# Optimization experiments

Measured on AMD Instinct MI355X. Metric: run time of the kernel, lower is better.

## Reference

```python
import jax, jax.numpy as jnp
import numpy as np
from jax import lax

K = 3          # kernel size
STRIDE = 1
PAD = 1
DIL = 1


def conv2d(x, w, b, stride, pad):
    y = lax.conv_general_dilated(
        x, w, (stride, stride), [(pad, pad), (pad, pad)],
        dimension_numbers=('NCHW', 'OIHW', 'NCHW'))
    return y + b[None, :, None, None]


def deform_conv2d(x, offset, mask, weight, bias):
    # x: [B,C,H,W]; offset: [B,2*K*K,Ho,Wo] (channel 2i = y_i, 2i+1 = x_i);
    # mask: [B,K*K,Ho,Wo]; weight: [Cout,C,K,K]  (deformable_groups=1, groups=1)
    B, C, H, W = x.shape
    Ho, Wo = offset.shape[2], offset.shape[3]
    KK = K * K
    off = offset.reshape(B, KK, 2, Ho, Wo)
    off_y, off_x = off[:, :, 0], off[:, :, 1]          # [B,KK,Ho,Wo]

    ky, kx = jnp.meshgrid(jnp.arange(K), jnp.arange(K), indexing='ij')
    ky, kx = ky.ravel(), kx.ravel()                    # [KK]
    base_y = (jnp.arange(Ho) * STRIDE - PAD)[None, :, None] + (ky * DIL)[:, None, None]
    base_x = (jnp.arange(Wo) * STRIDE - PAD)[None, None, :] + (kx * DIL)[:, None, None]
    py = base_y[None].astype(x.dtype) + off_y          # [B,KK,Ho,Wo]
    px = base_x[None].astype(x.dtype) + off_x

    y0 = jnp.floor(py)
    x0 = jnp.floor(px)
    ly = py - y0
    lx = px - x0
    y0i = y0.astype(jnp.int32)
    x0i = x0.astype(jnp.int32)
    y1i = y0i + 1
    x1i = x0i + 1

    x_flat = x.reshape(B, C, H * W)

    def gather(yi, xi):
        valid = (yi >= 0) & (yi < H) & (xi >= 0) & (xi < W)
        idx = jnp.clip(yi, 0, H - 1) * W + jnp.clip(xi, 0, W - 1)
        v = jax.vmap(lambda xb, ib: xb[:, ib])(x_flat, idx.reshape(B, -1))
        v = v.reshape(B, C, KK, Ho, Wo)
        return v * valid[:, None].astype(x.dtype)

    w00 = ((1 - ly) * (1 - lx))[:, None]
    w01 = ((1 - ly) * lx)[:, None]
    w10 = (ly * (1 - lx))[:, None]
    w11 = (ly * lx)[:, None]
    samp = (w00 * gather(y0i, x0i) + w01 * gather(y0i, x1i)
            + w10 * gather(y1i, x0i) + w11 * gather(y1i, x1i))  # [B,C,KK,Ho,Wo]

    mod = samp * mask[:, None]                          # modulated samples
    wr = weight.reshape(weight.shape[0], C, KK)
    out = jnp.einsum('ocp,bcphw->bohw', wr, mod)
    return out + bias[None, :, None, None]


def setup_inputs() -> dict:
    key = jax.random.key(0)
    k1, k2, k3, k4, k5 = jax.random.split(key, 5)
    B, Cin, Cout, H, W = 4, 64, 128, 128, 128
    x = jax.random.normal(k1, (B, Cin, H, W), dtype=jnp.float32)
    # offset/mask conv: 3*K*K channels (o1, o2, mask). Zero-init in the source;
    # small random values here so nonzero offsets exercise the gather.
    offset_w = jax.random.normal(k2, (3 * K * K, Cin, K, K), dtype=jnp.float32) * 0.01
    offset_b = jax.random.normal(k3, (3 * K * K,), dtype=jnp.float32) * 0.01
    weight = jax.random.normal(k4, (Cout, Cin, K, K), dtype=jnp.float32) * (1.0 / np.sqrt(Cin * K * K))
    bias = jax.random.normal(k5, (Cout,), dtype=jnp.float32) * 0.01
    return {'x': x, 'offset_w': offset_w, 'offset_b': offset_b, 'weight': weight, 'bias': bias}


def reference(x, offset_w, offset_b, weight, bias):
    out = conv2d(x, offset_w, offset_b, STRIDE, PAD)    # [B,3*KK,Ho,Wo]
    o1, o2, m = jnp.split(out, 3, axis=1)
    offset = jnp.concatenate([o1, o2], axis=1)          # [B,2*KK,Ho,Wo]
    mask = jax.nn.sigmoid(m)                            # [B,KK,Ho,Wo]
    return deform_conv2d(x, offset, mask, weight, bias)
```

## Files before the change

### kernel.cpp

```cpp
#include <hip/hip_runtime.h>
#include <math.h>

#define HH   128
#define WW   128
#define HWP  16384
#define CIN  64
#define COUT 128

typedef float  f32x4  __attribute__((ext_vector_type(4)));
typedef short  short8 __attribute__((ext_vector_type(8)));

#define WBF_B   ((size_t)0)
#define OWBF_B  ((size_t)147456)
#define XT_B    ((size_t)221184)
#define WS_NEED ((size_t)8609792)

__device__ inline unsigned short f2bf(float f) {
    unsigned u = __builtin_bit_cast(unsigned, f);
    return (unsigned short)((u + 0x7FFFu + ((u >> 16) & 1u)) >> 16);
}

__global__ __launch_bounds__(256) void k_prep(const float* __restrict__ x,
                                              const float* __restrict__ wgt,
                                              const float* __restrict__ ow,
                                              unsigned short* __restrict__ xt,
                                              unsigned short* __restrict__ wbf,
                                              unsigned short* __restrict__ owbf) {
    int t = threadIdx.x;
    if (blockIdx.x < 2048) {
        int cgrp = t & 7, px = t >> 3;
        int pix = blockIdx.x * 32 + px;
        int b = pix >> 14, hw = pix & 16383;
        const float* xp = x + (size_t)b * CIN * HWP + (size_t)(cgrp * 8) * HWP + hw;
        unsigned pk[4];
#pragma unroll
        for (int d = 0; d < 4; ++d) {
            float lo = xp[(size_t)(2 * d) * HWP];
            float hi = xp[(size_t)(2 * d + 1) * HWP];
            pk[d] = (unsigned)f2bf(lo) | ((unsigned)f2bf(hi) << 16);
        }
        *(uint4*)(xt + (size_t)pix * 64 + cgrp * 8) = *(uint4*)pk;
    } else {
        int tid = (blockIdx.x - 2048) * 256 + t;
        {
            int oc = tid / 576;
            int r  = tid - oc * 576;
            int kk = r >> 6;
            int c  = r & 63;
            wbf[tid] = f2bf(wgt[((size_t)oc * CIN + c) * 9 + kk]);
        }
        if (tid < 32 * 576) {
            int oc  = tid / 576;
            int r   = tid - oc * 576;
            int tap = r >> 6;
            int c   = r & 63;
            owbf[tid] = (oc < 27) ? f2bf(ow[((size_t)oc * CIN + c) * 9 + tap]) : 0;
        }
    }
}

__global__ __launch_bounds__(256) void k_fused_v2(const unsigned short* __restrict__ xt,
                                                  const unsigned short* __restrict__ wbf,
                                                  const unsigned short* __restrict__ owbf,
                                                  const float* __restrict__ ob,
                                                  const float* __restrict__ bias,
                                                  float* __restrict__ out) {
    __shared__ __align__(16) char smem[11648];
    char*  mbase  = smem;
    float* meta_s = (float*)(smem + 8192);

    int blk0 = blockIdx.x;
    int blk  = (blk0 & 7) * 256 + (blk0 >> 3);
    int b   = blk >> 9;
    int rem = blk & 511;
    int h   = rem >> 2;
    int w0  = (rem & 3) << 5;
    int t   = threadIdx.x;

    int p1 = t >> 3;
    int cg = t & 7;
    int l  = t & 63;
    int wid = t >> 6;
    int lm = l & 15, lk = l >> 4;

    const unsigned short* xbt = xt + (size_t)b * HWP * 64;

    int ocf = wid >> 1, pxf = wid & 1;
    int spx = pxf * 16 + lm;
    f32x4 sacc = {0.f, 0.f, 0.f, 0.f};
    const unsigned short* sab = owbf + (size_t)(ocf * 16 + lm) * 576 + lk * 8;

#pragma unroll
    for (int tap = 0; tap < 9; ++tap) {
        int ky = tap / 3, kx = tap % 3;
        int yy = h - 1 + ky;
        int xx = w0 - 1 + kx + spx;
        bool vld = (yy >= 0) && (yy < HH) && (xx >= 0) && (xx < WW);
        int yc = min(max(yy, 0), HH - 1), xc = min(max(xx, 0), WW - 1);
        const unsigned short* bp = xbt + (size_t)(yc * WW + xc) * 64 + lk * 8;
#pragma unroll
        for (int ch = 0; ch < 2; ++ch) {
            short8 a = *(const short8*)(sab + tap * 64 + ch * 32);
            uint4 v = *(const uint4*)(bp + ch * 32);
            v.x = vld ? v.x : 0u;  v.y = vld ? v.y : 0u;
            v.z = vld ? v.z : 0u;  v.w = vld ? v.w : 0u;
            sacc = __builtin_amdgcn_mfma_f32_16x16x32_bf16(a, __builtin_bit_cast(short8, v), sacc, 0, 0, 0);
        }
    }
#pragma unroll
    for (int r = 0; r < 4; ++r) {
        int oc = ocf * 16 + lk * 4 + r;
        if (oc < 27) {
            float v = sacc[r] + ob[oc];
            if (oc < 18) {
                meta_s[(oc & 1) * 288 + (oc >> 1) * 32 + spx] = v;
            } else {
                meta_s[2 * 288 + (oc - 18) * 32 + spx] = 1.f / (1.f + expf(-v));
            }
        }
    }
    __syncthreads();

    f32x4 acc00 = {0.f,0.f,0.f,0.f};
    f32x4 acc01 = {0.f,0.f,0.f,0.f};
    f32x4 acc10 = {0.f,0.f,0.f,0.f};
    f32x4 acc11 = {0.f,0.f,0.f,0.f};

    const unsigned short* arow0 = wbf + (size_t)(wid * 32 + lm) * 576 + lk * 8;
    const unsigned short* arow1 = arow0 + 16 * 576;

    int pA = lm, pB = lm + 16;
    int rbA = pA * 128, rbB = pB * 128;
    int swA = pA & 7,   swB = pB & 7;

    uint4 cc00, cc01, cc10, cc11;
    float cw00, cw01, cw10, cw11;

    const unsigned short* xbc = xbt + cg * 8;

#define PREF_CORNERS(KK) do {                                                  \
      int ky_ = (KK) / 3, kx_ = (KK) % 3;                                      \
      float offy = meta_s[(KK) * 32 + p1];                                     \
      float offx = meta_s[288 + (KK) * 32 + p1];                               \
      float msk  = meta_s[576 + (KK) * 32 + p1];                               \
      float py = (float)(h - 1 + ky_) + offy;                                  \
      float px = (float)(w0 + p1 - 1 + kx_) + offx;                            \
      float y0f = floorf(py), x0f = floorf(px);                                \
      float ly = py - y0f, lx = px - x0f;                                      \
      int y0 = (int)y0f, x0i = (int)x0f;                                       \
      int y1 = y0 + 1, x1 = x0i + 1;                                           \
      bool vy0 = (y0 >= 0) && (y0 < HH);                                       \
      bool vy1 = (y1 >= 0) && (y1 < HH);                                       \
      bool vx0 = (x0i >= 0) && (x0i < WW);                                     \
      bool vx1 = (x1 >= 0) && (x1 < WW);                                       \
      int yc0 = min(max(y0, 0), HH - 1), yc1 = min(max(y1, 0), HH - 1);        \
      int xc0 = min(max(x0i, 0), WW - 1), xc1 = min(max(x1, 0), WW - 1);       \
      cw00 = (1.f - ly) * (1.f - lx) * ((vy0 && vx0) ? msk : 0.f);             \
      cw01 = (1.f - ly) * lx         * ((vy0 && vx1) ? msk : 0.f);             \
      cw10 = ly * (1.f - lx)         * ((vy1 && vx0) ? msk : 0.f);             \
      cw11 = ly * lx                 * ((vy1 && vx1) ? msk : 0.f);             \
      cc00 = *(const uint4*)(xbc + (size_t)(yc0 * WW + xc0) * 64);             \
      cc01 = *(const uint4*)(xbc + (size_t)(yc0 * WW + xc1) * 64);             \
      cc10 = *(const uint4*)(xbc + (size_t)(yc1 * WW + xc0) * 64);             \
      cc11 = *(const uint4*)(xbc + (size_t)(yc1 * WW + xc1) * 64);             \
    } while (0)

    PREF_CORNERS(0);

#pragma unroll
    for (int kk = 0; kk < 9; ++kk) {
        const int cur = kk & 1;
        {
            char* wdst = mbase + cur * 4096;
            unsigned pk[4];
#pragma unroll
            for (int d = 0; d < 4; ++d) {
                unsigned u0 = (&cc00.x)[d], u1 = (&cc01.x)[d];
                unsigned u2 = (&cc10.x)[d], u3 = (&cc11.x)[d];
                float lo = cw00 * __builtin_bit_cast(float, u0 << 16)
                         + cw01 * __builtin_bit_cast(float, u1 << 16)
                         + cw10 * __builtin_bit_cast(float, u2 << 16)
                         + cw11 * __builtin_bit_cast(float, u3 << 16);
                float hi = cw00 * __builtin_bit_cast(float, u0 & 0xFFFF0000u)
                         + cw01 * __builtin_bit_cast(float, u1 & 0xFFFF0000u)
                         + cw10 * __builtin_bit_cast(float, u2 & 0xFFFF0000u)
                         + cw11 * __builtin_bit_cast(float, u3 & 0xFFFF0000u);
                pk[d] = (unsigned)f2bf(lo) | ((unsigned)f2bf(hi) << 16);
            }
            *(uint4*)(wdst + p1 * 128 + (((unsigned)(cg ^ (p1 & 7))) << 4)) = *(uint4*)pk;
        }

        if (kk < 8) PREF_CORNERS(kk + 1);

        asm volatile("s_waitcnt lgkmcnt(0)" ::: "memory");
        __builtin_amdgcn_s_barrier();
        __builtin_amdgcn_sched_barrier(0);

        const char* rb = mbase + cur * 4096;
#pragma unroll
        for (int sstep = 0; sstep < 2; ++sstep) {
            short8 a0 = *(const short8*)(arow0 + kk * 64 + sstep * 32);
            short8 a1 = *(const short8*)(arow1 + kk * 64 + sstep * 32);
            int kb = sstep * 4 + lk;
            short8 b0 = *(const short8*)(rb + rbA + ((kb ^ swA) << 4));
            short8 b1 = *(const short8*)(rb + rbB + ((kb ^ swB) << 4));
            acc00 = __builtin_amdgcn_mfma_f32_16x16x32_bf16(a0, b0, acc00, 0, 0, 0);
            acc01 = __builtin_amdgcn_mfma_f32_16x16x32_bf16(a0, b1, acc01, 0, 0, 0);
            acc10 = __builtin_amdgcn_mfma_f32_16x16x32_bf16(a1, b0, acc10, 0, 0, 0);
            acc11 = __builtin_amdgcn_mfma_f32_16x16x32_bf16(a1, b1, acc11, 0, 0, 0);
        }
    }
#undef PREF_CORNERS

    size_t outb = (size_t)b * COUT * HWP + (size_t)h * WW + w0;
#pragma unroll
    for (int of = 0; of < 2; ++of) {
        f32x4 aP = of ? acc10 : acc00;
        f32x4 aQ = of ? acc11 : acc01;
        int ocb = wid * 32 + of * 16 + lk * 4;
#pragma unroll
        for (int r = 0; r < 4; ++r) {
            int oc = ocb + r;
            float bi = bias[oc];
            out[outb + (size_t)oc * HWP + pA] = aP[r] + bi;
            out[outb + (size_t)oc * HWP + pB] = aQ[r] + bi;
        }
    }
}

__global__ __launch_bounds__(256) void k_fused_v1(const float* __restrict__ x,
                                                  const unsigned short* __restrict__ wbf,
                                                  const unsigned short* __restrict__ owbf,
                                                  const float* __restrict__ ob,
                                                  const float* __restrict__ bias,
                                                  float* __restrict__ out) {
    __shared__ __align__(16) char smem[16768];
    char*  ctx    = smem;
    char*  mbase  = smem;
    float* meta_s = (float*)(smem + 13312);

    int blk = blockIdx.x;
    int b   = blk >> 9;
    int rem = blk & 511;
    int h   = rem >> 2;
    int w0  = (rem & 3) << 5;
    int t   = threadIdx.x;

    int p1 = t & 31;
    int cg = t >> 5;
    int l  = t & 63;
    int wid = t >> 6;
    int lm = l & 15, lk = l >> 4;

    const float* xb = x + (size_t)b * CIN * HWP;

#pragma unroll
    for (int c = 0; c < 4; ++c) {
        int j = c * 256 + t;
        if (j < 816) {
            int g   = j / 34;
            int px  = j - g * 34;
            int row = g >> 3;
            int cgj = g & 7;
            int yy = h - 1 + row;
            int xx = w0 - 1 + px;
            bool vld = (yy >= 0) && (yy < HH) && (xx >= 0) && (xx < WW);
            int  sidx = vld ? (yy * WW + xx) : 0;
            float s[8];
#pragma unroll
            for (int i = 0; i < 8; ++i)
                s[i] = vld ? xb[(size_t)(cgj * 8 + i) * HWP + sidx] : 0.f;
            uint4 pk;
            pk.x = (unsigned)f2bf(s[0]) | ((unsigned)f2bf(s[1]) << 16);
            pk.y = (unsigned)f2bf(s[2]) | ((unsigned)f2bf(s[3]) << 16);
            pk.z = (unsigned)f2bf(s[4]) | ((unsigned)f2bf(s[5]) << 16);
            pk.w = (unsigned)f2bf(s[6]) | ((unsigned)f2bf(s[7]) << 16);
            *(uint4*)(ctx + (row * 34 + px) * 128 + ((cgj ^ (px & 7)) << 4)) = pk;
        }
    }
    __syncthreads();

    int ocf = wid >> 1, pxf = wid & 1;
    int spx = pxf * 16 + lm;
    f32x4 sacc = {0.f, 0.f, 0.f, 0.f};
    const unsigned short* sab = owbf + (size_t)(ocf * 16 + lm) * 576 + lk * 8;

#pragma unroll
    for (int tap = 0; tap < 9; ++tap) {
        int ky = tap / 3, kx = tap % 3;
        int cpx = kx + spx;
        int crb = (ky * 34 + cpx) * 128;
        int csw = cpx & 7;
#pragma unroll
        for (int ch = 0; ch < 2; ++ch) {
            short8 a  = *(const short8*)(sab + tap * 64 + ch * 32);
            int kb = ch * 4 + lk;
            short8 bf = *(const short8*)(ctx + crb + (((unsigned)(kb ^ csw)) << 4));
            sacc = __builtin_amdgcn_mfma_f32_16x16x32_bf16(a, bf, sacc, 0, 0, 0);
        }
    }
#pragma unroll
    for (int r = 0; r < 4; ++r) {
        int oc = ocf * 16 + lk * 4 + r;
        if (oc < 27) {
            float v = sacc[r] + ob[oc];
            if (oc < 18) {
                meta_s[(oc & 1) * 288 + (oc >> 1) * 32 + spx] = v;
            } else {
                meta_s[2 * 288 + (oc - 18) * 32 + spx] = 1.f / (1.f + expf(-v));
            }
        }
    }
    __syncthreads();

    f32x4 acc00 = {0.f,0.f,0.f,0.f};
    f32x4 acc01 = {0.f,0.f,0.f,0.f};
    f32x4 acc10 = {0.f,0.f,0.f,0.f};
    f32x4 acc11 = {0.f,0.f,0.f,0.f};

    const unsigned short* arow0 = wbf + (size_t)(wid * 32 + lm) * 576 + lk * 8;
    const unsigned short* arow1 = arow0 + 16 * 576;

    int pA = lm, pB = lm + 16;
    int rbA = pA * 128, rbB = pB * 128;
    int swA = pA & 7,   swB = pB & 7;

    float  cw00, cw01, cw10, cw11;
    float  cc00[8], cc01[8], cc10[8], cc11[8];
    short8 na0[2], na1[2];

#define PREF_CORNERS(KK) do {                                                  \
      int ky = (KK) / 3, kx = (KK) % 3;                                        \
      float offy = meta_s[(KK) * 32 + p1];                                     \
      float offx = meta_s[288 + (KK) * 32 + p1];                               \
      float msk  = meta_s[576 + (KK) * 32 + p1];                               \
      float py = (float)(h - 1 + ky) + offy;                                   \
      float px = (float)(w0 + p1 - 1 + kx) + offx;                             \
      float y0f = floorf(py), x0f = floorf(px);                                \
      float ly = py - y0f, lx = px - x0f;                                      \
      int y0 = (int)y0f, x0i = (int)x0f;                                       \
      int y1 = y0 + 1, x1 = x0i + 1;                                           \
      bool vy0 = (y0 >= 0) && (y0 < HH);                                       \
      bool vy1 = (y1 >= 0) && (y1 < HH);                                       \
      bool vx0 = (x0i >= 0) && (x0i < WW);                                     \
      bool vx1 = (x1 >= 0) && (x1 < WW);                                       \
      int yc0 = min(max(y0, 0), HH - 1), yc1 = min(max(y1, 0), HH - 1);        \
      int xc0 = min(max(x0i, 0), WW - 1), xc1 = min(max(x1, 0), WW - 1);       \
      cw00 = (1.f - ly) * (1.f - lx) * ((vy0 && vx0) ? msk : 0.f);             \
      cw01 = (1.f - ly) * lx         * ((vy0 && vx1) ? msk : 0.f);             \
      cw10 = ly * (1.f - lx)         * ((vy1 && vx0) ? msk : 0.f);             \
      cw11 = ly * lx                 * ((vy1 && vx1) ? msk : 0.f);             \
      int idx00 = yc0 * WW + xc0, idx01 = yc0 * WW + xc1;                      \
      int idx10 = yc1 * WW + xc0, idx11 = yc1 * WW + xc1;                      \
      const float* basec = xb + (size_t)(cg * 8) * HWP;                        \
      _Pragma("unroll")                                                        \
      for (int i = 0; i < 8; ++i) {                                            \
        const float* bc = basec + (size_t)i * HWP;                             \
        cc00[i] = bc[idx00]; cc01[i] = bc[idx01];                              \
        cc10[i] = bc[idx10]; cc11[i] = bc[idx11];                              \
      }                                                                        \
    } while (0)

#define PREF_AFRAG(KK) do {                                                    \
      na0[0] = *(const short8*)(arow0 + (KK) * 64);                            \
      na0[1] = *(const short8*)(arow0 + (KK) * 64 + 32);                       \
      na1[0] = *(const short8*)(arow1 + (KK) * 64);                            \
      na1[1] = *(const short8*)(arow1 + (KK) * 64 + 32);                       \
    } while (0)

    PREF_CORNERS(0);
    PREF_AFRAG(0);

#pragma unroll
    for (int kk = 0; kk < 9; ++kk) {
        {
            char* wdst = mbase + (kk & 1) * 4096;
            float s[8];
#pragma unroll
            for (int i = 0; i < 8; ++i)
                s[i] = cw00 * cc00[i] + cw01 * cc01[i]
                     + cw10 * cc10[i] + cw11 * cc11[i];
            uint4 pk;
            pk.x = (unsigned)f2bf(s[0]) | ((unsigned)f2bf(s[1]) << 16);
            pk.y = (unsigned)f2bf(s[2]) | ((unsigned)f2bf(s[3]) << 16);
            pk.z = (unsigned)f2bf(s[4]) | ((unsigned)f2bf(s[5]) << 16);
            pk.w = (unsigned)f2bf(s[6]) | ((unsigned)f2bf(s[7]) << 16);
            *(uint4*)(wdst + p1 * 128 + (((unsigned)(cg ^ (p1 & 7))) << 4)) = pk;
        }
        if (kk < 8) PREF_CORNERS(kk + 1);
        asm volatile("s_waitcnt lgkmcnt(0)" ::: "memory");
        __builtin_amdgcn_s_barrier();
        __builtin_amdgcn_sched_barrier(0);
        const char* rb = mbase + (kk & 1) * 4096;
#pragma unroll
        for (int sstep = 0; sstep < 2; ++sstep) {
            short8 a0 = na0[sstep];
            short8 a1 = na1[sstep];
            int kb = sstep * 4 + lk;
            short8 b0 = *(const short8*)(rb + rbA + ((kb ^ swA) << 4));
            short8 b1 = *(const short8*)(rb + rbB + ((kb ^ swB) << 4));
            acc00 = __builtin_amdgcn_mfma_f32_16x16x32_bf16(a0, b0, acc00, 0, 0, 0);
            acc01 = __builtin_amdgcn_mfma_f32_16x16x32_bf16(a0, b1, acc01, 0, 0, 0);
            acc10 = __builtin_amdgcn_mfma_f32_16x16x32_bf16(a1, b0, acc10, 0, 0, 0);
            acc11 = __builtin_amdgcn_mfma_f32_16x16x32_bf16(a1, b1, acc11, 0, 0, 0);
        }
        if (kk < 8) PREF_AFRAG(kk + 1);
    }
#undef PREF_CORNERS
#undef PREF_AFRAG

    size_t outb = (size_t)b * COUT * HWP + (size_t)h * WW + w0;
#pragma unroll
    for (int of = 0; of < 2; ++of) {
        f32x4 aP = of ? acc10 : acc00;
        f32x4 aQ = of ? acc11 : acc01;
        int ocb = wid * 32 + of * 16 + lk * 4;
#pragma unroll
        for (int r = 0; r < 4; ++r) {
            int oc = ocb + r;
            float bi = bias[oc];
            out[outb + (size_t)oc * HWP + pA] = aP[r] + bi;
            out[outb + (size_t)oc * HWP + pB] = aQ[r] + bi;
        }
    }
}

extern "C" void kernel_launch(void* const* d_in, const int* in_sizes, int n_in,
                              void* d_out, int out_size, void* d_ws, size_t ws_size,
                              hipStream_t stream) {
    const float* x    = (const float*)d_in[0];
    const float* ow   = (const float*)d_in[1];
    const float* ob   = (const float*)d_in[2];
    const float* wgt  = (const float*)d_in[3];
    const float* bias = (const float*)d_in[4];
    float* out = (float*)d_out;
    char* ws = (char*)d_ws;

    unsigned short* wbf  = (unsigned short*)(ws + WBF_B);
    unsigned short* owbf = (unsigned short*)(ws + OWBF_B);
    unsigned short* xt   = (unsigned short*)(ws + XT_B);

    if (ws_size >= WS_NEED) {
        hipLaunchKernelGGL(k_prep, dim3(2336), dim3(256), 0, stream,
                           x, wgt, ow, xt, wbf, owbf);
        hipLaunchKernelGGL(k_fused_v2, dim3(2048), dim3(256), 0, stream,
                           xt, wbf, owbf, ob, bias, out);
    } else {
        hipLaunchKernelGGL(k_prep, dim3(2336), dim3(256), 0, stream,
                           x, wgt, ow, xt, wbf, owbf);
        hipLaunchKernelGGL(k_fused_v1, dim3(2048), dim3(256), 0, stream,
                           x, wbf, owbf, ob, bias, out);
    }
}
```

Measured before the change: 92.34 us.

## Process two kernel taps per barrier with double-width prefetch and four LDS buffers

Restructures the 9-tap loop so that each iteration gathers and writes two taps' bilinear samples into separate LDS buffers before one barrier, then runs MFMAs for both. The goal is to halve the barrier count and put more gather loads in flight to hide memory latency. In exchange, LDS per block grows to about 19.8 KB and corner-register pressure doubles, which may reduce occupancy.

```diff
diff --git a/kernel.cpp b/kernel.cpp
--- a/kernel.cpp
+++ b/kernel.cpp
@@ -65,9 +65,9 @@
                                                   const float* __restrict__ ob,
                                                   const float* __restrict__ bias,
                                                   float* __restrict__ out) {
-    __shared__ __align__(16) char smem[11648];
+    __shared__ __align__(16) char smem[19840];
     char*  mbase  = smem;
-    float* meta_s = (float*)(smem + 8192);
+    float* meta_s = (float*)(smem + 16384);
 
     int blk0 = blockIdx.x;
     int blk  = (blk0 & 7) * 256 + (blk0 >> 3);
@@ -133,12 +133,12 @@
     int rbA = pA * 128, rbB = pB * 128;
     int swA = pA & 7,   swB = pB & 7;
 
-    uint4 cc00, cc01, cc10, cc11;
-    float cw00, cw01, cw10, cw11;
+    uint4 ccA0, ccA1, ccA2, ccA3, ccB0, ccB1, ccB2, ccB3;
+    float cwA0, cwA1, cwA2, cwA3, cwB0, cwB1, cwB2, cwB3;
 
     const unsigned short* xbc = xbt + cg * 8;
 
-#define PREF_CORNERS(KK) do {                                                  \
+#define PREF_C(KK, C0, C1, C2, C3, W0, W1, W2, W3) do {                        \
       int ky_ = (KK) / 3, kx_ = (KK) % 3;                                      \
       float offy = meta_s[(KK) * 32 + p1];                                     \
       float offx = meta_s[288 + (KK) * 32 + p1];                               \
@@ -155,62 +155,85 @@
       bool vx1 = (x1 >= 0) && (x1 < WW);                                       \
       int yc0 = min(max(y0, 0), HH - 1), yc1 = min(max(y1, 0), HH - 1);        \
       int xc0 = min(max(x0i, 0), WW - 1), xc1 = min(max(x1, 0), WW - 1);       \
-      cw00 = (1.f - ly) * (1.f - lx) * ((vy0 && vx0) ? msk : 0.f);             \
-      cw01 = (1.f - ly) * lx         * ((vy0 && vx1) ? msk : 0.f);             \
-      cw10 = ly * (1.f - lx)         * ((vy1 && vx0) ? msk : 0.f);             \
-      cw11 = ly * lx                 * ((vy1 && vx1) ? msk : 0.f);             \
-      cc00 = *(const uint4*)(xbc + (size_t)(yc0 * WW + xc0) * 64);             \
-      cc01 = *(const uint4*)(xbc + (size_t)(yc0 * WW + xc1) * 64);             \
-      cc10 = *(const uint4*)(xbc + (size_t)(yc1 * WW + xc0) * 64);             \
-      cc11 = *(const uint4*)(xbc + (size_t)(yc1 * WW + xc1) * 64);             \
+      W0 = (1.f - ly) * (1.f - lx) * ((vy0 && vx0) ? msk : 0.f);               \
+      W1 = (1.f - ly) * lx         * ((vy0 && vx1) ? msk : 0.f);               \
+      W2 = ly * (1.f - lx)         * ((vy1 && vx0) ? msk : 0.f);               \
+      W3 = ly * lx                 * ((vy1 && vx1) ? msk : 0.f);               \
+      C0 = *(const uint4*)(xbc + (size_t)(yc0 * WW + xc0) * 64);               \
+      C1 = *(const uint4*)(xbc + (size_t)(yc0 * WW + xc1) * 64);               \
+      C2 = *(const uint4*)(xbc + (size_t)(yc1 * WW + xc0) * 64);               \
+      C3 = *(const uint4*)(xbc + (size_t)(yc1 * WW + xc1) * 64);               \
     } while (0)
 
-    PREF_CORNERS(0);
-
-#pragma unroll
-    for (int kk = 0; kk < 9; ++kk) {
-        const int cur = kk & 1;
-        {
-            char* wdst = mbase + cur * 4096;
-            unsigned pk[4];
-#pragma unroll
-            for (int d = 0; d < 4; ++d) {
-                unsigned u0 = (&cc00.x)[d], u1 = (&cc01.x)[d];
-                unsigned u2 = (&cc10.x)[d], u3 = (&cc11.x)[d];
-                float lo = cw00 * __builtin_bit_cast(float, u0 << 16)
-                         + cw01 * __builtin_bit_cast(float, u1 << 16)
-                         + cw10 * __builtin_bit_cast(float, u2 << 16)
-                         + cw11 * __builtin_bit_cast(float, u3 << 16);
-                float hi = cw00 * __builtin_bit_cast(float, u0 & 0xFFFF0000u)
-                         + cw01 * __builtin_bit_cast(float, u1 & 0xFFFF0000u)
-                         + cw10 * __builtin_bit_cast(float, u2 & 0xFFFF0000u)
-                         + cw11 * __builtin_bit_cast(float, u3 & 0xFFFF0000u);
-                pk[d] = (unsigned)f2bf(lo) | ((unsigned)f2bf(hi) << 16);
-            }
-            *(uint4*)(wdst + p1 * 128 + (((unsigned)(cg ^ (p1 & 7))) << 4)) = *(uint4*)pk;
-        }
-
-        if (kk < 8) PREF_CORNERS(kk + 1);
+#define COMB_W(DST, C0, C1, C2, C3, W0, W1, W2, W3) do {                       \
+      unsigned pk[4];                                                          \
+      _Pragma("unroll")                                                        \
+      for (int d = 0; d < 4; ++d) {                                            \
+          unsigned u0 = (&(C0).x)[d], u1 = (&(C1).x)[d];                       \
+          unsigned u2 = (&(C2).x)[d], u3 = (&(C3).x)[d];                       \
+          float lo = (W0) * __builtin_bit_cast(float, u0 << 16)                \
+                   + (W1) * __builtin_bit_cast(float, u1 << 16)                \
+                   + (W2) * __builtin_bit_cast(float, u2 << 16)                \
+                   + (W3) * __builtin_bit_cast(float, u3 << 16);               \
+          float hi = (W0) * __builtin_bit_cast(float, u0 & 0xFFFF0000u)        \
+                   + (W1) * __builtin_bit_cast(float, u1 & 0xFFFF0000u)        \
+                   + (W2) * __builtin_bit_cast(float, u2 & 0xFFFF0000u)        \
+                   + (W3) * __builtin_bit_cast(float, u3 & 0xFFFF0000u);       \
+          pk[d] = (unsigned)f2bf(lo) | ((unsigned)f2bf(hi) << 16);             \
+      }                                                                        \
+      *(uint4*)((DST) + p1 * 128 + (((unsigned)(cg ^ (p1 & 7))) << 4)) = *(uint4*)pk; \
+    } while (0)
+
+#define MFMA_TILE(RB, KK) do {                                                 \
+      _Pragma("unroll")                                                        \
+      for (int sstep = 0; sstep < 2; ++sstep) {                                \
+          short8 a0 = *(const short8*)(arow0 + (KK) * 64 + sstep * 32);        \
+          short8 a1 = *(const short8*)(arow1 + (KK) * 64 + sstep * 32);        \
+          int kb = sstep * 4 + lk;                                             \
+          short8 b0 = *(const short8*)((RB) + rbA + ((kb ^ swA) << 4));        \
+          short8 b1 = *(const short8*)((RB) + rbB + ((kb ^ swB) << 4));        \
+          acc00 = __builtin_amdgcn_mfma_f32_16x16x32_bf16(a0, b0, acc00, 0, 0, 0); \
+          acc01 = __builtin_amdgcn_mfma_f32_16x16x32_bf16(a0, b1, acc01, 0, 0, 0); \
+          acc10 = __builtin_amdgcn_mfma_f32_16x16x32_bf16(a1, b0, acc10, 0, 0, 0); \
+          acc11 = __builtin_amdgcn_mfma_f32_16x16x32_bf16(a1, b1, acc11, 0, 0, 0); \
+      }                                                                        \
+    } while (0)
+
+    PREF_C(0, ccA0, ccA1, ccA2, ccA3, cwA0, cwA1, cwA2, cwA3);
+    PREF_C(1, ccB0, ccB1, ccB2, ccB3, cwB0, cwB1, cwB2, cwB3);
+
+#pragma unroll
+    for (int r = 0; r < 4; ++r) {
+        char* d0 = mbase + ((r & 1) * 2 + 0) * 4096;
+        char* d1 = mbase + ((r & 1) * 2 + 1) * 4096;
+        COMB_W(d0, ccA0, ccA1, ccA2, ccA3, cwA0, cwA1, cwA2, cwA3);
+        COMB_W(d1, ccB0, ccB1, ccB2, ccB3, cwB0, cwB1, cwB2, cwB3);
+
+        if (r < 3) {
+            PREF_C(2 * r + 2, ccA0, ccA1, ccA2, ccA3, cwA0, cwA1, cwA2, cwA3);
+            PREF_C(2 * r + 3, ccB0, ccB1, ccB2, ccB3, cwB0, cwB1, cwB2, cwB3);
+        } else {
+            PREF_C(8, ccA0, ccA1, ccA2, ccA3, cwA0, cwA1, cwA2, cwA3);
+        }
 
         asm volatile("s_waitcnt lgkmcnt(0)" ::: "memory");
         __builtin_amdgcn_s_barrier();
         __builtin_amdgcn_sched_barrier(0);
 
-        const char* rb = mbase + cur * 4096;
-#pragma unroll
-        for (int sstep = 0; sstep < 2; ++sstep) {
-            short8 a0 = *(const short8*)(arow0 + kk * 64 + sstep * 32);
-            short8 a1 = *(const short8*)(arow1 + kk * 64 + sstep * 32);
-            int kb = sstep * 4 + lk;
-            short8 b0 = *(const short8*)(rb + rbA + ((kb ^ swA) << 4));
-            short8 b1 = *(const short8*)(rb + rbB + ((kb ^ swB) << 4));
-            acc00 = __builtin_amdgcn_mfma_f32_16x16x32_bf16(a0, b0, acc00, 0, 0, 0);
-            acc01 = __builtin_amdgcn_mfma_f32_16x16x32_bf16(a0, b1, acc01, 0, 0, 0);
-            acc10 = __builtin_amdgcn_mfma_f32_16x16x32_bf16(a1, b0, acc10, 0, 0, 0);
-            acc11 = __builtin_amdgcn_mfma_f32_16x16x32_bf16(a1, b1, acc11, 0, 0, 0);
-        }
-    }
-#undef PREF_CORNERS
+        MFMA_TILE(d0, 2 * r);
+        MFMA_TILE(d1, 2 * r + 1);
+    }
+    {
+        char* d0 = mbase;
+        COMB_W(d0, ccA0, ccA1, ccA2, ccA3, cwA0, cwA1, cwA2, cwA3);
+        asm volatile("s_waitcnt lgkmcnt(0)" ::: "memory");
+        __builtin_amdgcn_s_barrier();
+        __builtin_amdgcn_sched_barrier(0);
+        MFMA_TILE(d0, 8);
+    }
+#undef PREF_C
+#undef COMB_W
+#undef MFMA_TILE
 
     size_t outb = (size_t)b * COUT * HWP + (size_t)h * WW + w0;
 #pragma unroll
```

Result: no change. 93.39 us (+1.1%).

## Split offset/mask conv into separate kernel writing fp16 metadata to workspace

Applied to the files above, without the earlier changes.

The offset/mask convolution moves out of the fused kernel into its own kernel, k_offc, which writes offsets and sigmoid masks as fp16 into a workspace buffer. The main deformable kernel then loads this metadata into shared memory instead of computing it. This takes the small-N MFMA offset conv out of the main kernel's critical path. In exchange it adds a kernel launch, an extra global round-trip of about 3.5MB, and fp16 precision on the offsets. The new path runs only when the workspace is at least WS_NEED3 bytes.

```diff
diff --git a/kernel.cpp b/kernel.cpp
--- a/kernel.cpp
+++ b/kernel.cpp
@@ -1,4 +1,5 @@
 #include <hip/hip_runtime.h>
+#include <hip/hip_fp16.h>
 #include <math.h>
 
 #define HH   128
@@ -10,10 +11,12 @@
 typedef float  f32x4  __attribute__((ext_vector_type(4)));
 typedef short  short8 __attribute__((ext_vector_type(8)));
 
-#define WBF_B   ((size_t)0)
-#define OWBF_B  ((size_t)147456)
-#define XT_B    ((size_t)221184)
-#define WS_NEED ((size_t)8609792)
+#define WBF_B    ((size_t)0)
+#define OWBF_B   ((size_t)147456)
+#define XT_B     ((size_t)221184)
+#define META_B   ((size_t)8609792)
+#define WS_NEED  ((size_t)8609792)
+#define WS_NEED3 ((size_t)12148736)
 
 __device__ inline unsigned short f2bf(float f) {
     unsigned u = __builtin_bit_cast(unsigned, f);
@@ -59,16 +62,10 @@
     }
 }
 
-__global__ __launch_bounds__(256) void k_fused_v2(const unsigned short* __restrict__ xt,
-                                                  const unsigned short* __restrict__ wbf,
-                                                  const unsigned short* __restrict__ owbf,
-                                                  const float* __restrict__ ob,
-                                                  const float* __restrict__ bias,
-                                                  float* __restrict__ out) {
-    __shared__ __align__(16) char smem[11648];
-    char*  mbase  = smem;
-    float* meta_s = (float*)(smem + 8192);
-
+__global__ __launch_bounds__(256) void k_offc(const unsigned short* __restrict__ xt,
+                                              const unsigned short* __restrict__ owbf,
+                                              const float* __restrict__ ob,
+                                              __half* __restrict__ meta_h) {
     int blk0 = blockIdx.x;
     int blk  = (blk0 & 7) * 256 + (blk0 >> 3);
     int b   = blk >> 9;
@@ -76,15 +73,11 @@
     int h   = rem >> 2;
     int w0  = (rem & 3) << 5;
     int t   = threadIdx.x;
-
-    int p1 = t >> 3;
-    int cg = t & 7;
-    int l  = t & 63;
+    int l   = t & 63;
     int wid = t >> 6;
-    int lm = l & 15, lk = l >> 4;
+    int lm  = l & 15, lk = l >> 4;
 
     const unsigned short* xbt = xt + (size_t)b * HWP * 64;
-
     int ocf = wid >> 1, pxf = wid & 1;
     int spx = pxf * 16 + lm;
     f32x4 sacc = {0.f, 0.f, 0.f, 0.f};
@@ -107,16 +100,53 @@
             sacc = __builtin_amdgcn_mfma_f32_16x16x32_bf16(a, __builtin_bit_cast(short8, v), sacc, 0, 0, 0);
         }
     }
+    int hw = h * WW + w0 + spx;
 #pragma unroll
     for (int r = 0; r < 4; ++r) {
         int oc = ocf * 16 + lk * 4 + r;
         if (oc < 27) {
             float v = sacc[r] + ob[oc];
-            if (oc < 18) {
-                meta_s[(oc & 1) * 288 + (oc >> 1) * 32 + spx] = v;
-            } else {
-                meta_s[2 * 288 + (oc - 18) * 32 + spx] = 1.f / (1.f + expf(-v));
-            }
+            int comp, kk;
+            if (oc < 18) { comp = oc & 1; kk = oc >> 1; }
+            else         { comp = 2; kk = oc - 18; v = 1.f / (1.f + expf(-v)); }
+            meta_h[((size_t)(comp * 9 + kk) * 4 + b) * HWP + hw] = __float2half(v);
+        }
+    }
+}
+
+__global__ __launch_bounds__(256) void k_main(const unsigned short* __restrict__ xt,
+                                              const unsigned short* __restrict__ wbf,
+                                              const __half* __restrict__ meta_h,
+                                              const float* __restrict__ bias,
+                                              float* __restrict__ out) {
+    __shared__ __align__(16) char smem[11648];
+    char*  mbase  = smem;
+    float* meta_s = (float*)(smem + 8192);
+
+    int blk0 = blockIdx.x;
+    int blk  = (blk0 & 7) * 256 + (blk0 >> 3);
+    int b   = blk >> 9;
+    int rem = blk & 511;
+    int h   = rem >> 2;
+    int w0  = (rem & 3) << 5;
+    int t   = threadIdx.x;
+
+    int p1 = t >> 3;
+    int cg = t & 7;
+    int l  = t & 63;
+    int wid = t >> 6;
+    int lm = l & 15, lk = l >> 4;
+
+    const unsigned short* xbt = xt + (size_t)b * HWP * 64;
+
+    {
+        int base_hw = h * WW + w0;
+        for (int j = t; j < 864; j += 256) {
+            int px = j & 31;
+            int ck = j >> 5;
+            float v = __half2float(meta_h[((size_t)ck * 4 + b) * HWP + base_hw + px]);
+            int comp = ck / 9, kk = ck - comp * 9;
+            meta_s[comp * 288 + kk * 32 + px] = v;
         }
     }
     __syncthreads();
@@ -189,13 +219,176 @@
             }
             *(uint4*)(wdst + p1 * 128 + (((unsigned)(cg ^ (p1 & 7))) << 4)) = *(uint4*)pk;
         }
-
         if (kk < 8) PREF_CORNERS(kk + 1);
-
         asm volatile("s_waitcnt lgkmcnt(0)" ::: "memory");
         __builtin_amdgcn_s_barrier();
         __builtin_amdgcn_sched_barrier(0);
-
+        const char* rb = mbase + cur * 4096;
+#pragma unroll
+        for (int sstep = 0; sstep < 2; ++sstep) {
+            short8 a0 = *(const short8*)(arow0 + kk * 64 + sstep * 32);
+            short8 a1 = *(const short8*)(arow1 + kk * 64 + sstep * 32);
+            int kb = sstep * 4 + lk;
+            short8 b0 = *(const short8*)(rb + rbA + ((kb ^ swA) << 4));
+            short8 b1 = *(const short8*)(rb + rbB + ((kb ^ swB) << 4));
+            acc00 = __builtin_amdgcn_mfma_f32_16x16x32_bf16(a0, b0, acc00, 0, 0, 0);
+            acc01 = __builtin_amdgcn_mfma_f32_16x16x32_bf16(a0, b1, acc01, 0, 0, 0);
+            acc10 = __builtin_amdgcn_mfma_f32_16x16x32_bf16(a1, b0, acc10, 0, 0, 0);
+            acc11 = __builtin_amdgcn_mfma_f32_16x16x32_bf16(a1, b1, acc11, 0, 0, 0);
+        }
+    }
+#undef PREF_CORNERS
+
+    size_t outb = (size_t)b * COUT * HWP + (size_t)h * WW + w0;
+#pragma unroll
+    for (int of = 0; of < 2; ++of) {
+        f32x4 aP = of ? acc10 : acc00;
+        f32x4 aQ = of ? acc11 : acc01;
+        int ocb = wid * 32 + of * 16 + lk * 4;
+#pragma unroll
+        for (int r = 0; r < 4; ++r) {
+            int oc = ocb + r;
+            float bi = bias[oc];
+            out[outb + (size_t)oc * HWP + pA] = aP[r] + bi;
+            out[outb + (size_t)oc * HWP + pB] = aQ[r] + bi;
+        }
+    }
+}
+
+__global__ __launch_bounds__(256) void k_fused_v2(const unsigned short* __restrict__ xt,
+                                                  const unsigned short* __restrict__ wbf,
+                                                  const unsigned short* __restrict__ owbf,
+                                                  const float* __restrict__ ob,
+                                                  const float* __restrict__ bias,
+                                                  float* __restrict__ out) {
+    __shared__ __align__(16) char smem[11648];
+    char*  mbase  = smem;
+    float* meta_s = (float*)(smem + 8192);
+
+    int blk0 = blockIdx.x;
+    int blk  = (blk0 & 7) * 256 + (blk0 >> 3);
+    int b   = blk >> 9;
+    int rem = blk & 511;
+    int h   = rem >> 2;
+    int w0  = (rem & 3) << 5;
+    int t   = threadIdx.x;
+
+    int p1 = t >> 3;
+    int cg = t & 7;
+    int l  = t & 63;
+    int wid = t >> 6;
+    int lm = l & 15, lk = l >> 4;
+
+    const unsigned short* xbt = xt + (size_t)b * HWP * 64;
+
+    int ocf = wid >> 1, pxf = wid & 1;
+    int spx = pxf * 16 + lm;
+    f32x4 sacc = {0.f, 0.f, 0.f, 0.f};
+    const unsigned short* sab = owbf + (size_t)(ocf * 16 + lm) * 576 + lk * 8;
+
+#pragma unroll
+    for (int tap = 0; tap < 9; ++tap) {
+        int ky = tap / 3, kx = tap % 3;
+        int yy = h - 1 + ky;
+        int xx = w0 - 1 + kx + spx;
+        bool vld = (yy >= 0) && (yy < HH) && (xx >= 0) && (xx < WW);
+        int yc = min(max(yy, 0), HH - 1), xc = min(max(xx, 0), WW - 1);
+        const unsigned short* bp = xbt + (size_t)(yc * WW + xc) * 64 + lk * 8;
+#pragma unroll
+        for (int ch = 0; ch < 2; ++ch) {
+            short8 a = *(const short8*)(sab + tap * 64 + ch * 32);
+            uint4 v = *(const uint4*)(bp + ch * 32);
+            v.x = vld ? v.x : 0u;  v.y = vld ? v.y : 0u;
+            v.z = vld ? v.z : 0u;  v.w = vld ? v.w : 0u;
+            sacc = __builtin_amdgcn_mfma_f32_16x16x32_bf16(a, __builtin_bit_cast(short8, v), sacc, 0, 0, 0);
+        }
+    }
+#pragma unroll
+    for (int r = 0; r < 4; ++r) {
+        int oc = ocf * 16 + lk * 4 + r;
+        if (oc < 27) {
+            float v = sacc[r] + ob[oc];
+            if (oc < 18) {
+                meta_s[(oc & 1) * 288 + (oc >> 1) * 32 + spx] = v;
+            } else {
+                meta_s[2 * 288 + (oc - 18) * 32 + spx] = 1.f / (1.f + expf(-v));
+            }
+        }
+    }
+    __syncthreads();
+
+    f32x4 acc00 = {0.f,0.f,0.f,0.f};
+    f32x4 acc01 = {0.f,0.f,0.f,0.f};
+    f32x4 acc10 = {0.f,0.f,0.f,0.f};
+    f32x4 acc11 = {0.f,0.f,0.f,0.f};
+
+    const unsigned short* arow0 = wbf + (size_t)(wid * 32 + lm) * 576 + lk * 8;
+    const unsigned short* arow1 = arow0 + 16 * 576;
+
+    int pA = lm, pB = lm + 16;
+    int rbA = pA * 128, rbB = pB * 128;
+    int swA = pA & 7,   swB = pB & 7;
+
+    uint4 cc00, cc01, cc10, cc11;
+    float cw00, cw01, cw10, cw11;
+
+    const unsigned short* xbc = xbt + cg * 8;
+
+#define PREF_CORNERS(KK) do {                                                  \
+      int ky_ = (KK) / 3, kx_ = (KK) % 3;                                      \
+      float offy = meta_s[(KK) * 32 + p1];                                     \
+      float offx = meta_s[288 + (KK) * 32 + p1];                               \
+      float msk  = meta_s[576 + (KK) * 32 + p1];                               \
+      float py = (float)(h - 1 + ky_) + offy;                                  \
+      float px = (float)(w0 + p1 - 1 + kx_) + offx;                            \
+      float y0f = floorf(py), x0f = floorf(px);                                \
+      float ly = py - y0f, lx = px - x0f;                                      \
+      int y0 = (int)y0f, x0i = (int)x0f;                                       \
+      int y1 = y0 + 1, x1 = x0i + 1;                                           \
+      bool vy0 = (y0 >= 0) && (y0 < HH);                                       \
+      bool vy1 = (y1 >= 0) && (y1 < HH);                                       \
+      bool vx0 = (x0i >= 0) && (x0i < WW);                                     \
+      bool vx1 = (x1 >= 0) && (x1 < WW);                                       \
+      int yc0 = min(max(y0, 0), HH - 1), yc1 = min(max(y1, 0), HH - 1);        \
+      int xc0 = min(max(x0i, 0), WW - 1), xc1 = min(max(x1, 0), WW - 1);       \
+      cw00 = (1.f - ly) * (1.f - lx) * ((vy0 && vx0) ? msk : 0.f);             \
+      cw01 = (1.f - ly) * lx         * ((vy0 && vx1) ? msk : 0.f);             \
+      cw10 = ly * (1.f - lx)         * ((vy1 && vx0) ? msk : 0.f);             \
+      cw11 = ly * lx                 * ((vy1 && vx1) ? msk : 0.f);             \
+      cc00 = *(const uint4*)(xbc + (size_t)(yc0 * WW + xc0) * 64);             \
+      cc01 = *(const uint4*)(xbc + (size_t)(yc0 * WW + xc1) * 64);             \
+      cc10 = *(const uint4*)(xbc + (size_t)(yc1 * WW + xc0) * 64);             \
+      cc11 = *(const uint4*)(xbc + (size_t)(yc1 * WW + xc1) * 64);             \
+    } while (0)
+
+    PREF_CORNERS(0);
+
+#pragma unroll
+    for (int kk = 0; kk < 9; ++kk) {
+        const int cur = kk & 1;
+        {
+            char* wdst = mbase + cur * 4096;
+            unsigned pk[4];
+#pragma unroll
+            for (int d = 0; d < 4; ++d) {
+                unsigned u0 = (&cc00.x)[d], u1 = (&cc01.x)[d];
+                unsigned u2 = (&cc10.x)[d], u3 = (&cc11.x)[d];
+                float lo = cw00 * __builtin_bit_cast(float, u0 << 16)
+                         + cw01 * __builtin_bit_cast(float, u1 << 16)
+                         + cw10 * __builtin_bit_cast(float, u2 << 16)
+                         + cw11 * __builtin_bit_cast(float, u3 << 16);
+                float hi = cw00 * __builtin_bit_cast(float, u0 & 0xFFFF0000u)
+                         + cw01 * __builtin_bit_cast(float, u1 & 0xFFFF0000u)
+                         + cw10 * __builtin_bit_cast(float, u2 & 0xFFFF0000u)
+                         + cw11 * __builtin_bit_cast(float, u3 & 0xFFFF0000u);
+                pk[d] = (unsigned)f2bf(lo) | ((unsigned)f2bf(hi) << 16);
+            }
+            *(uint4*)(wdst + p1 * 128 + (((unsigned)(cg ^ (p1 & 7))) << 4)) = *(uint4*)pk;
+        }
+        if (kk < 8) PREF_CORNERS(kk + 1);
+        asm volatile("s_waitcnt lgkmcnt(0)" ::: "memory");
+        __builtin_amdgcn_s_barrier();
+        __builtin_amdgcn_sched_barrier(0);
         const char* rb = mbase + cur * 4096;
 #pragma unroll
         for (int sstep = 0; sstep < 2; ++sstep) {
@@ -439,15 +632,19 @@
     unsigned short* wbf  = (unsigned short*)(ws + WBF_B);
     unsigned short* owbf = (unsigned short*)(ws + OWBF_B);
     unsigned short* xt   = (unsigned short*)(ws + XT_B);
-
-    if (ws_size >= WS_NEED) {
-        hipLaunchKernelGGL(k_prep, dim3(2336), dim3(256), 0, stream,
-                           x, wgt, ow, xt, wbf, owbf);
+    __half*         mh   = (__half*)(ws + META_B);
+
+    hipLaunchKernelGGL(k_prep, dim3(2336), dim3(256), 0, stream,
+                       x, wgt, ow, xt, wbf, owbf);
+    if (ws_size >= WS_NEED3) {
+        hipLaunchKernelGGL(k_offc, dim3(2048), dim3(256), 0, stream,
+                           xt, owbf, ob, mh);
+        hipLaunchKernelGGL(k_main, dim3(2048), dim3(256), 0, stream,
+                           xt, wbf, mh, bias, out);
+    } else if (ws_size >= WS_NEED) {
         hipLaunchKernelGGL(k_fused_v2, dim3(2048), dim3(256), 0, stream,
                            xt, wbf, owbf, ob, bias, out);
     } else {
-        hipLaunchKernelGGL(k_prep, dim3(2336), dim3(256), 0, stream,
-                           x, wgt, ow, xt, wbf, owbf);
         hipLaunchKernelGGL(k_fused_v1, dim3(2048), dim3(256), 0, stream,
                            x, wbf, owbf, ob, bias, out);
     }
```

After: 96.07 us. +4.0%, slower.
